# Kernel optimization log

Measured on AMD Instinct MI355X. Metric: run time of the kernel, lower is better.

Reference implementation:

```python
import jax, jax.numpy as jnp
import numpy as np

N_NODES = 16384
D_IN = 256
D_OUT = 256
AVG_DEG = 32


def setup_inputs() -> dict:
    key = jax.random.key(0)
    kx, ka, kw, kb = jax.random.split(key, 4)
    x = jax.random.normal(kx, (N_NODES, D_IN), dtype=jnp.float32)
    # Binary dense adjacency with average degree ~AVG_DEG (matches `adj[i] > 0` usage).
    adj = (jax.random.uniform(ka, (N_NODES, N_NODES)) < (AVG_DEG / N_NODES)).astype(jnp.float32)
    # nn.Linear(2*in_features, out_features): weight [out, 2*in], bias [out]
    W = jax.random.normal(kw, (D_OUT, 2 * D_IN), dtype=jnp.float32) * (1.0 / np.sqrt(2 * D_IN))
    b = jnp.zeros((D_OUT,), dtype=jnp.float32)
    return {"x": x, "adj": adj, "W": W, "b": b, "sample_size": 10}


def reference(x, adj, W, b, sample_size):
    # Vectorized equivalent of the per-node loop:
    # sample min(deg, sample_size) neighbors uniformly without replacement,
    # mean-aggregate, concat with self features, linear + relu.
    key = jax.random.key(42)
    noise = jax.random.uniform(key, adj.shape)            # [N, N]
    # Gumbel-top-k trick: top-k uniform scores over neighbors == uniform sample w/o replacement.
    scores = jnp.where(adj > 0, noise, -jnp.inf)
    top_scores, top_idx = jax.lax.top_k(scores, sample_size)  # [N, k]
    valid = jnp.isfinite(top_scores)                          # [N, k] false where deg < k
    feats = x[top_idx] * valid[..., None].astype(x.dtype)     # [N, k, d]
    cnt = valid.sum(axis=-1, keepdims=True).astype(x.dtype)   # [N, 1]
    agg = feats.sum(axis=1) / jnp.maximum(cnt, 1.0)           # mean; zeros if no neighbors
    h = jnp.concatenate([x, agg], axis=-1)                    # [N, 2d]
    return jax.nn.relu(h @ W.T + b)
```

## Files before the change

### kernel.cpp

```cpp
#include <hip/hip_runtime.h>
#include <hip/hip_bf16.h>
#include <stdint.h>

#define N_NODES 16384
#define D_IN    256
#define D_OUT   256
#define K_SAMP  10
#define HALF_FLAT (1u << 27)

#define NPB 32
#define NPW 4

#define JAX_PARTITIONABLE 1

typedef __attribute__((ext_vector_type(4))) float  f32x4;
typedef __attribute__((ext_vector_type(8))) short  bf16x8;
typedef __attribute__((ext_vector_type(4))) int    i32x4;

__device__ __forceinline__ uint32_t rotl32(uint32_t x, int r) {
    return (x << r) | (x >> (32 - r));
}

__device__ __forceinline__ uint32_t jax_noise_bits(uint32_t r, uint32_t c) {
    const uint32_t i  = (r << 14) | c;
    const uint32_t k0 = 0u, k1 = 42u;
    const uint32_t k2 = 42u ^ 0x1BD11BDAu;
    uint32_t x0, x1;
#if JAX_PARTITIONABLE
    x0 = 0u;
    x1 = i;
#else
    const bool lo = (i < HALF_FLAT);
    x0 = lo ? i : (i - HALF_FLAT);
    x1 = lo ? (i + HALF_FLAT) : i;
#endif
    x0 += k0; x1 += k1;
#define TFR4(a,b,cc,d) \
    x0 += x1; x1 = rotl32(x1,a);  x1 ^= x0; \
    x0 += x1; x1 = rotl32(x1,b);  x1 ^= x0; \
    x0 += x1; x1 = rotl32(x1,cc); x1 ^= x0; \
    x0 += x1; x1 = rotl32(x1,d);  x1 ^= x0;
    TFR4(13,15,26,6);   x0 += k1; x1 += k2 + 1u;
    TFR4(17,29,16,24);  x0 += k2; x1 += k0 + 2u;
    TFR4(13,15,26,6);   x0 += k0; x1 += k1 + 3u;
    TFR4(17,29,16,24);  x0 += k1; x1 += k2 + 4u;
    TFR4(13,15,26,6);   x0 += k2; x1 += k0 + 5u;
#undef TFR4
#if JAX_PARTITIONABLE
    return x0 ^ x1;
#else
    return (i < HALF_FLAT) ? x0 : x1;
#endif
}

__device__ __forceinline__ unsigned short f2bfbits(float f) {
    __hip_bfloat16 h = __float2bfloat16(f);
    return *(unsigned short*)&h;
}

__global__ __launch_bounds__(256) void k_convw(const float* __restrict__ W,
                                               unsigned short* __restrict__ Wb)
{
    int i = (blockIdx.x * 256 + threadIdx.x) * 4;
    f32x4 v = *(const f32x4*)(W + i);
    ushort4 u;
    u.x = f2bfbits(v[0]); u.y = f2bfbits(v[1]);
    u.z = f2bfbits(v[2]); u.w = f2bfbits(v[3]);
    *(ushort4*)(Wb + i) = u;
}

__global__ __launch_bounds__(512, 4) void k_fused(
    const float* __restrict__ x, const float* __restrict__ adj,
    const unsigned short* __restrict__ Wb, const float* __restrict__ bias,
    float* __restrict__ out)
{
    __shared__ short hS[NPB * 512];
    __shared__ short Bs[256 * 64];
    unsigned short* candc = (unsigned short*)Bs;

    const int t    = threadIdx.x;
    const int lane = t & 63;
    const int w    = t >> 6;

    for (int i = 0; i < NPW; ++i) {
        const int lrow = w * NPW + i;
        const int r    = blockIdx.x * NPB + lrow;

        const i32x4* rowp = (const i32x4*)(adj + (size_t)r * N_NODES);
        int nc = 0;
        #pragma unroll 8
        for (int it = 0; it < 64; ++it) {
            i32x4 v = __builtin_nontemporal_load(rowp + it * 64 + lane);
            uint32_t any = (uint32_t)v[0] | (uint32_t)v[1] | (uint32_t)v[2] | (uint32_t)v[3];
            if (__ballot(any != 0u)) {
                int cb = (it * 64 + lane) * 4;
                #pragma unroll
                for (int j = 0; j < 4; ++j) {
                    unsigned long long mask = __ballot(v[j] != 0);
                    if (mask) {
                        if (v[j] != 0) {
                            int below = __builtin_amdgcn_mbcnt_hi(
                                (uint32_t)(mask >> 32),
                                __builtin_amdgcn_mbcnt_lo((uint32_t)mask, 0));
                            int slot = nc + below;
                            if (slot < 128) candc[w * 128 + slot] = (unsigned short)(cb + j);
                        }
                        nc += __popcll(mask);
                    }
                }
            }
        }
        if (nc > 128) nc = 128;

        unsigned long long k0 = 0ull, k1 = 0ull;
        if (lane < nc) {
            uint32_t c   = candc[w * 128 + lane];
            uint32_t u23 = jax_noise_bits((uint32_t)r, c) >> 9;
            k0 = ((((unsigned long long)u23) << 14) | (unsigned long long)(16383u - c)) + 1ull;
        }
        if (64 + lane < nc) {
            uint32_t c   = candc[w * 128 + 64 + lane];
            uint32_t u23 = jax_noise_bits((uint32_t)r, c) >> 9;
            k1 = ((((unsigned long long)u23) << 14) | (unsigned long long)(16383u - c)) + 1ull;
        }

        const int m = nc < K_SAMP ? nc : K_SAMP;
        int cols[K_SAMP];
        #pragma unroll
        for (int s = 0; s < K_SAMP; ++s) {
            unsigned long long my = k0 > k1 ? k0 : k1;
            #pragma unroll
            for (int o = 1; o < 64; o <<= 1) {
                unsigned long long other = __shfl_xor(my, o);
                if (other > my) my = other;
            }
            if (k0 == my) k0 = 0ull; else if (k1 == my) k1 = 0ull;
            cols[s] = 16383 - (int)((my - 1ull) & 0x3FFFull);
        }
        f32x4 acc = {0.f, 0.f, 0.f, 0.f};
        #pragma unroll
        for (int s = 0; s < K_SAMP; ++s) {
            const float wt = (s < m) ? 1.0f : 0.0f;
            f32x4 xv = *(const f32x4*)(x + (size_t)cols[s] * D_IN + lane * 4);
            acc += wt * xv;
        }
        const float inv = (m > 0) ? 1.0f / (float)m : 0.0f;

        f32x4 sv = *(const f32x4*)(x + (size_t)r * D_IN + lane * 4);
        ushort4 us, ua;
        us.x = f2bfbits(sv[0]);        us.y = f2bfbits(sv[1]);
        us.z = f2bfbits(sv[2]);        us.w = f2bfbits(sv[3]);
        ua.x = f2bfbits(acc[0] * inv); ua.y = f2bfbits(acc[1] * inv);
        ua.z = f2bfbits(acc[2] * inv); ua.w = f2bfbits(acc[3] * inv);
        const int swz = (lrow & 7) << 4;
        *(ushort4*)((char*)hS + ((lrow * 1024 + lane * 8) ^ swz))       = us;
        *(ushort4*)((char*)hS + ((lrow * 1024 + 512 + lane * 8) ^ swz)) = ua;
    }

    __syncthreads();

    const int wm = w >> 2;
    const int wn = w & 3;
    const int lr = lane & 15;
    const int lk = lane >> 4;

    f32x4 acc[4] = {};

    int srow[4], sc16[4], sba[4];
    #pragma unroll
    for (int i2 = 0; i2 < 4; ++i2) {
        int q = t + i2 * 512;
        srow[i2] = q >> 3; sc16[i2] = q & 7;
        sba[i2]  = (srow[i2] * 128 + sc16[i2] * 16) ^ ((srow[i2] & 7) << 4);
    }

    i32x4 breg[4];
    #pragma unroll
    for (int i2 = 0; i2 < 4; ++i2)
        breg[i2] = *(const i32x4*)(Wb + (size_t)srow[i2] * 512 + sc16[i2] * 8);

    for (int cc = 0; cc < 8; ++cc) {
        #pragma unroll
        for (int i2 = 0; i2 < 4; ++i2)
            *(i32x4*)((char*)Bs + sba[i2]) = breg[i2];
        __syncthreads();

        if (cc < 7) {
            const int kb = (cc + 1) * 64;
            #pragma unroll
            for (int i2 = 0; i2 < 4; ++i2)
                breg[i2] = *(const i32x4*)(Wb + (size_t)srow[i2] * 512 + kb + sc16[i2] * 8);
        }

        #pragma unroll
        for (int kk = 0; kk < 64; kk += 32) {
            const int arow = wm * 16 + lr;
            const int aba  = (arow * 1024 + cc * 128 + kk * 2 + lk * 16) ^ ((arow & 7) << 4);
            bf16x8 af = *(const bf16x8*)((const char*)hS + aba);
            #pragma unroll
            for (int ni = 0; ni < 4; ++ni) {
                const int n  = wn * 64 + ni * 16 + lr;
                const int bb = (n * 128 + kk * 2 + lk * 16) ^ ((n & 7) << 4);
                bf16x8 bf = *(const bf16x8*)((const char*)Bs + bb);
                acc[ni] = __builtin_amdgcn_mfma_f32_16x16x32_bf16(af, bf, acc[ni], 0, 0, 0);
            }
        }
        __syncthreads();
    }

    #pragma unroll
    for (int ni = 0; ni < 4; ++ni) {
        const int col = wn * 64 + ni * 16 + lr;
        const float bv = bias[col];
        #pragma unroll
        for (int j = 0; j < 4; ++j) {
            const int rowg = blockIdx.x * NPB + wm * 16 + lk * 4 + j;
            float v = acc[ni][j] + bv;
            v = v > 0.0f ? v : 0.0f;
            __builtin_nontemporal_store(v, out + (size_t)rowg * D_OUT + col);
        }
    }
}

extern "C" void kernel_launch(void* const* d_in, const int* in_sizes, int n_in,
                              void* d_out, int out_size, void* d_ws, size_t ws_size,
                              hipStream_t stream) {
    (void)in_sizes; (void)n_in; (void)out_size; (void)ws_size;
    const float* x   = (const float*)d_in[0];
    const float* adj = (const float*)d_in[1];
    const float* W   = (const float*)d_in[2];
    const float* b   = (const float*)d_in[3];

    unsigned short* Wb = (unsigned short*)d_ws;
    float* out = (float*)d_out;

    hipLaunchKernelGGL(k_convw, dim3(128), dim3(256), 0, stream, W, Wb);
    hipLaunchKernelGGL(k_fused, dim3(N_NODES / NPB), dim3(512), 0, stream,
                       x, adj, Wb, b, out);
}
```

Before: 215.9 us.

## Halve rows per block, read W fragments from global, loop sampling only m times

Blocks now process 16 rows with 256 threads, doubling the grid and removing the 512-thread launch bound. The GEMM stage no longer stages W tiles in LDS with barriers; each wave reads bf16 W fragments directly from global/L2. The neighbor-selection loop runs only m iterations and gathers inline, skipping the masked extra loads. This cuts LDS use and synchronization but increases global/L2 traffic for W and reduces reuse of W per block.

```diff
diff --git a/kernel.cpp b/kernel.cpp
--- a/kernel.cpp
+++ b/kernel.cpp
@@ -8,7 +8,7 @@
 #define K_SAMP  10
 #define HALF_FLAT (1u << 27)
 
-#define NPB 32
+#define NPB 16
 #define NPW 4
 
 #define JAX_PARTITIONABLE 1
@@ -69,14 +69,13 @@
     *(ushort4*)(Wb + i) = u;
 }
 
-__global__ __launch_bounds__(512, 4) void k_fused(
+__global__ __launch_bounds__(256) void k_fused(
     const float* __restrict__ x, const float* __restrict__ adj,
     const unsigned short* __restrict__ Wb, const float* __restrict__ bias,
     float* __restrict__ out)
 {
     __shared__ short hS[NPB * 512];
-    __shared__ short Bs[256 * 64];
-    unsigned short* candc = (unsigned short*)Bs;
+    __shared__ unsigned short candc[4][128];
 
     const int t    = threadIdx.x;
     const int lane = t & 63;
@@ -103,7 +102,7 @@
                                 (uint32_t)(mask >> 32),
                                 __builtin_amdgcn_mbcnt_lo((uint32_t)mask, 0));
                             int slot = nc + below;
-                            if (slot < 128) candc[w * 128 + slot] = (unsigned short)(cb + j);
+                            if (slot < 128) candc[w][slot] = (unsigned short)(cb + j);
                         }
                         nc += __popcll(mask);
                     }
@@ -114,20 +113,19 @@
 
         unsigned long long k0 = 0ull, k1 = 0ull;
         if (lane < nc) {
-            uint32_t c   = candc[w * 128 + lane];
+            uint32_t c   = candc[w][lane];
             uint32_t u23 = jax_noise_bits((uint32_t)r, c) >> 9;
             k0 = ((((unsigned long long)u23) << 14) | (unsigned long long)(16383u - c)) + 1ull;
         }
         if (64 + lane < nc) {
-            uint32_t c   = candc[w * 128 + 64 + lane];
+            uint32_t c   = candc[w][64 + lane];
             uint32_t u23 = jax_noise_bits((uint32_t)r, c) >> 9;
             k1 = ((((unsigned long long)u23) << 14) | (unsigned long long)(16383u - c)) + 1ull;
         }
 
         const int m = nc < K_SAMP ? nc : K_SAMP;
-        int cols[K_SAMP];
-        #pragma unroll
-        for (int s = 0; s < K_SAMP; ++s) {
+        f32x4 acc = {0.f, 0.f, 0.f, 0.f};
+        for (int s = 0; s < m; ++s) {
             unsigned long long my = k0 > k1 ? k0 : k1;
             #pragma unroll
             for (int o = 1; o < 64; o <<= 1) {
@@ -135,14 +133,9 @@
                 if (other > my) my = other;
             }
             if (k0 == my) k0 = 0ull; else if (k1 == my) k1 = 0ull;
-            cols[s] = 16383 - (int)((my - 1ull) & 0x3FFFull);
-        }
-        f32x4 acc = {0.f, 0.f, 0.f, 0.f};
-        #pragma unroll
-        for (int s = 0; s < K_SAMP; ++s) {
-            const float wt = (s < m) ? 1.0f : 0.0f;
-            f32x4 xv = *(const f32x4*)(x + (size_t)cols[s] * D_IN + lane * 4);
-            acc += wt * xv;
+            const int col = 16383 - (int)((my - 1ull) & 0x3FFFull);
+            f32x4 xv = *(const f32x4*)(x + (size_t)col * D_IN + lane * 4);
+            acc += xv;
         }
         const float inv = (m > 0) ? 1.0f / (float)m : 0.0f;
 
@@ -159,53 +152,22 @@
 
     __syncthreads();
 
-    const int wm = w >> 2;
-    const int wn = w & 3;
+    const int wn = w;
     const int lr = lane & 15;
     const int lk = lane >> 4;
 
     f32x4 acc[4] = {};
 
-    int srow[4], sc16[4], sba[4];
-    #pragma unroll
-    for (int i2 = 0; i2 < 4; ++i2) {
-        int q = t + i2 * 512;
-        srow[i2] = q >> 3; sc16[i2] = q & 7;
-        sba[i2]  = (srow[i2] * 128 + sc16[i2] * 16) ^ ((srow[i2] & 7) << 4);
-    }
-
-    i32x4 breg[4];
-    #pragma unroll
-    for (int i2 = 0; i2 < 4; ++i2)
-        breg[i2] = *(const i32x4*)(Wb + (size_t)srow[i2] * 512 + sc16[i2] * 8);
-
-    for (int cc = 0; cc < 8; ++cc) {
+    #pragma unroll 4
+    for (int kk = 0; kk < 512; kk += 32) {
+        const int aba = (lr * 1024 + kk * 2 + lk * 16) ^ ((lr & 7) << 4);
+        bf16x8 af = *(const bf16x8*)((const char*)hS + aba);
         #pragma unroll
-        for (int i2 = 0; i2 < 4; ++i2)
-            *(i32x4*)((char*)Bs + sba[i2]) = breg[i2];
-        __syncthreads();
-
-        if (cc < 7) {
-            const int kb = (cc + 1) * 64;
-            #pragma unroll
-            for (int i2 = 0; i2 < 4; ++i2)
-                breg[i2] = *(const i32x4*)(Wb + (size_t)srow[i2] * 512 + kb + sc16[i2] * 8);
-        }
-
-        #pragma unroll
-        for (int kk = 0; kk < 64; kk += 32) {
-            const int arow = wm * 16 + lr;
-            const int aba  = (arow * 1024 + cc * 128 + kk * 2 + lk * 16) ^ ((arow & 7) << 4);
-            bf16x8 af = *(const bf16x8*)((const char*)hS + aba);
-            #pragma unroll
-            for (int ni = 0; ni < 4; ++ni) {
-                const int n  = wn * 64 + ni * 16 + lr;
-                const int bb = (n * 128 + kk * 2 + lk * 16) ^ ((n & 7) << 4);
-                bf16x8 bf = *(const bf16x8*)((const char*)Bs + bb);
-                acc[ni] = __builtin_amdgcn_mfma_f32_16x16x32_bf16(af, bf, acc[ni], 0, 0, 0);
-            }
-        }
-        __syncthreads();
+        for (int ni = 0; ni < 4; ++ni) {
+            const int n = wn * 64 + ni * 16 + lr;
+            bf16x8 bf = *(const bf16x8*)(Wb + (size_t)n * 512 + kk + lk * 8);
+            acc[ni] = __builtin_amdgcn_mfma_f32_16x16x32_bf16(af, bf, acc[ni], 0, 0, 0);
+        }
     }
 
     #pragma unroll
@@ -214,7 +176,7 @@
         const float bv = bias[col];
         #pragma unroll
         for (int j = 0; j < 4; ++j) {
-            const int rowg = blockIdx.x * NPB + wm * 16 + lk * 4 + j;
+            const int rowg = blockIdx.x * NPB + lk * 4 + j;
             float v = acc[ni][j] + bv;
             v = v > 0.0f ? v : 0.0f;
             __builtin_nontemporal_store(v, out + (size_t)rowg * D_OUT + col);
@@ -235,6 +197,6 @@
     float* out = (float*)d_out;
 
     hipLaunchKernelGGL(k_convw, dim3(128), dim3(256), 0, stream, W, Wb);
-    hipLaunchKernelGGL(k_fused, dim3(N_NODES / NPB), dim3(512), 0, stream,
+    hipLaunchKernelGGL(k_fused, dim3(N_NODES / NPB), dim3(256), 0, stream,
                        x, adj, Wb, b, out);
 }
```

Result: slower. 241.8 us (+12.0%).
